# Performance work log

Hardware: AMD Instinct MI355X
Metric: run time of the kernel (lower is better)

The kernel has to match this reference:

```python
import jax, jax.numpy as jnp
import numpy as np

B, T, D = 2, 2048, 1024
H = 16
DH = D // H


def setup_inputs() -> dict:
    key = jax.random.key(0)
    ks = jax.random.split(key, 6)
    s = 1.0 / np.sqrt(D)
    return {
        "x": jax.random.normal(ks[0], (B, T, D), dtype=jnp.float32),
        "Wq": jax.random.normal(ks[1], (D, D), dtype=jnp.float32) * s,
        "Wk": jax.random.normal(ks[2], (D, D), dtype=jnp.float32) * s,
        "Wv": jax.random.normal(ks[3], (D, D), dtype=jnp.float32) * s,
        "Wo": jax.random.normal(ks[4], (D, D), dtype=jnp.float32) * s,
        "bo": jax.random.normal(ks[5], (D,), dtype=jnp.float32) * s,
    }


def reference(x, Wq, Wk, Wv, Wo, bo):
    b, t, _ = x.shape
    # separate Q/K/V projections (nn.Linear: x @ W.T, no bias)
    q = (x @ Wq.T).reshape(b, t, H, DH).transpose(0, 2, 1, 3)  # [b,h,t,hd]
    k = (x @ Wk.T).reshape(b, t, H, DH).transpose(0, 2, 1, 3)
    v = (x @ Wv.T).reshape(b, t, H, DH).transpose(0, 2, 1, 3)

    scores = jnp.einsum("bhqd,bhkd->bhqk", q, k)  # [b,h,t,t]
    causal = jnp.triu(jnp.ones((t, t), dtype=bool), k=1)
    scores = jnp.where(causal, -jnp.inf, scores)
    weights = jax.nn.softmax(scores / np.sqrt(DH), axis=-1)
    # dropout p=0.0 -> identity
    ctx = jnp.einsum("bhqk,bhkd->bhqd", weights, v)  # [b,h,t,hd]
    # NOTE: original code reshapes WITHOUT transposing heads back — replicate faithfully
    ctx = ctx.reshape(b, t, H * DH)
    return ctx @ Wo.T + bo
```

## Files before the change

### kernel.cpp

```cpp
#include <hip/hip_runtime.h>
#include <math.h>

#define BATCH 2
#define SEQ   2048
#define DIM   1024
#define NH    16
#define HD    64
#define MTOT  4096

typedef __attribute__((ext_vector_type(8)))  short bf16x8;
typedef __attribute__((ext_vector_type(4)))  float f32x4;
typedef __attribute__((ext_vector_type(16))) float f32x16;

__device__ __forceinline__ ushort f2bf(float f) {
    union { float f; unsigned u; } v; v.f = f;
    unsigned r = v.u + 0x7fffu + ((v.u >> 16) & 1u);
    return (ushort)(r >> 16);
}

__device__ __forceinline__ unsigned cvtpk_bf16(float lo, float hi) {
    unsigned r;
    asm("v_cvt_pk_bf16_f32 %0, %1, %2" : "=v"(r) : "v"(lo), "v"(hi));
    return r;
}

__global__ __launch_bounds__(256)
void cast_all(const float* __restrict__ x,
              const float* __restrict__ Wq, const float* __restrict__ Wk,
              const float* __restrict__ Wv, const float* __restrict__ Wo,
              ushort* __restrict__ xb,
              ushort* __restrict__ wqb, ushort* __restrict__ wkb,
              ushort* __restrict__ wvb, ushort* __restrict__ wob)
{
    const int z = blockIdx.y;
    const float* s; ushort* d; int n4;
    if (z == 0)      { s = x;  d = xb;  n4 = MTOT * DIM / 4; }
    else if (z == 1) { s = Wq; d = wqb; n4 = DIM * DIM / 4; }
    else if (z == 2) { s = Wk; d = wkb; n4 = DIM * DIM / 4; }
    else if (z == 3) { s = Wv; d = wvb; n4 = DIM * DIM / 4; }
    else             { s = Wo; d = wob; n4 = DIM * DIM / 4; }
    for (int i = blockIdx.x * blockDim.x + threadIdx.x; i < n4;
         i += gridDim.x * blockDim.x) {
        float4 v = ((const float4*)s)[i];
        ushort4 o;
        o.x = f2bf(v.x); o.y = f2bf(v.y); o.z = f2bf(v.z); o.w = f2bf(v.w);
        ((ushort4*)d)[i] = o;
    }
}

template<int MODE>
__global__ __launch_bounds__(256)
void gemm_bf16(const ushort* __restrict__ A,
               const ushort* __restrict__ W0, const ushort* __restrict__ W1,
               const ushort* __restrict__ W2,
               ushort* __restrict__ D0, ushort* __restrict__ D1,
               ushort* __restrict__ D2,
               const float* __restrict__ bias, float* __restrict__ Fout)
{
    __shared__ __align__(16) ushort As[2][128 * 64];
    __shared__ __align__(16) ushort Bs[2][128 * 64];

    const int tid = threadIdx.x;
    const int w = tid >> 6, l = tid & 63;
    const int g = l >> 4, l15 = l & 15;
    const int wr = w >> 1, wc = w & 1;
    const int brow = blockIdx.x * 128, bcol = blockIdx.y * 128;

    const ushort* W = (MODE == 1) ? W0
                    : (blockIdx.z == 0 ? W0 : (blockIdx.z == 1 ? W1 : W2));
    ushort* Dst = (MODE == 1) ? (ushort*)0
                : (blockIdx.z == 0 ? D0 : (blockIdx.z == 1 ? D1 : D2));

    const int rsub = l >> 3;
    const int gc   = ((l & 7) ^ rsub) * 8;
    const size_t arow0 = (size_t)(brow + 32 * w + rsub) * DIM;
    const size_t brow0 = (size_t)(bcol + 32 * w + rsub) * DIM;

    auto STAGE = [&](int buf, int ktel) {
        #pragma unroll
        for (int i = 0; i < 4; ++i) {
            __builtin_amdgcn_global_load_lds(
                (const __attribute__((address_space(1))) void*)
                    &A[arow0 + (size_t)(8 * i) * DIM + ktel + gc],
                (__attribute__((address_space(3))) void*)
                    &As[buf][(32 * w + 8 * i) * 64], 16, 0, 0);
            __builtin_amdgcn_global_load_lds(
                (const __attribute__((address_space(1))) void*)
                    &W[brow0 + (size_t)(8 * i) * DIM + ktel + gc],
                (__attribute__((address_space(3))) void*)
                    &Bs[buf][(32 * w + 8 * i) * 64], 16, 0, 0);
        }
    };

    STAGE(0, 0);
    STAGE(1, 64);

    f32x4 acc[4][4] = {};

    for (int t = 0; t < 16; ++t) {
        const int cur = t & 1;
        if (t < 15) asm volatile("s_waitcnt vmcnt(8)" ::: "memory");
        else        asm volatile("s_waitcnt vmcnt(0)" ::: "memory");
        __builtin_amdgcn_s_barrier();
        __builtin_amdgcn_sched_barrier(0);

        #pragma unroll
        for (int kh = 0; kh < 2; ++kh) {
            bf16x8 af[4], bfr[4];
            #pragma unroll
            for (int mi = 0; mi < 4; ++mi) {
                int row = 64 * wr + 16 * mi + l15;
                af[mi] = *(const bf16x8*)&As[cur][row * 64 + (((4 * kh + g) ^ (row & 7)) * 8)];
            }
            #pragma unroll
            for (int nj = 0; nj < 4; ++nj) {
                int row = 64 * wc + 16 * nj + l15;
                bfr[nj] = *(const bf16x8*)&Bs[cur][row * 64 + (((4 * kh + g) ^ (row & 7)) * 8)];
            }
            __builtin_amdgcn_s_setprio(1);
            #pragma unroll
            for (int mi = 0; mi < 4; ++mi)
                #pragma unroll
                for (int nj = 0; nj < 4; ++nj)
                    acc[mi][nj] = __builtin_amdgcn_mfma_f32_16x16x32_bf16(
                        af[mi], bfr[nj], acc[mi][nj], 0, 0, 0);
            __builtin_amdgcn_s_setprio(0);
        }

        __builtin_amdgcn_sched_barrier(0);
        __builtin_amdgcn_s_barrier();
        if (t + 2 < 16) STAGE(cur, (t + 2) * 64);
    }

    if (MODE == 0) {
        const float osc = (blockIdx.z == 0) ? 0.125f : 1.0f;
        if (blockIdx.z == 2) {
            #pragma unroll
            for (int mi = 0; mi < 4; ++mi)
                #pragma unroll
                for (int nj = 0; nj < 4; ++nj)
                    #pragma unroll
                    for (int reg = 0; reg < 4; ++reg) {
                        int row = brow + 64 * wr + 16 * mi + 4 * g + reg;
                        int col = bcol + 64 * wc + 16 * nj + l15;
                        int b = row >> 11, t = row & (SEQ - 1);
                        int hh = col >> 6, hd = col & 63;
                        Dst[(size_t)(b * NH + hh) * SEQ * HD
                            + ((size_t)(t >> 3) * 64 + hd) * 8 + (t & 7)] =
                            f2bf(acc[mi][nj][reg]);
                    }
        } else {
            #pragma unroll
            for (int mi = 0; mi < 4; ++mi)
                #pragma unroll
                for (int nj = 0; nj < 4; ++nj)
                    #pragma unroll
                    for (int reg = 0; reg < 4; ++reg) {
                        int row = brow + 64 * wr + 16 * mi + 4 * g + reg;
                        int col = bcol + 64 * wc + 16 * nj + l15;
                        int b = row >> 11, t = row & (SEQ - 1);
                        int hh = col >> 6, hd = col & 63;
                        Dst[(size_t)(b * NH + hh) * SEQ * HD
                            + (((size_t)(t >> 5) * 8 + (hd >> 3)) * 32 + (t & 31)) * 8
                            + (hd & 7)] = f2bf(acc[mi][nj][reg] * osc);
                    }
        }
    } else {
        #pragma unroll
        for (int nj = 0; nj < 4; ++nj) {
            int col = bcol + 64 * wc + 16 * nj + l15;
            float bv = bias[col];
            #pragma unroll
            for (int mi = 0; mi < 4; ++mi)
                #pragma unroll
                for (int reg = 0; reg < 4; ++reg) {
                    int row = brow + 64 * wr + 16 * mi + 4 * g + reg;
                    Fout[(size_t)row * DIM + col] = acc[mi][nj][reg] + bv;
                }
        }
    }
}

__global__ __launch_bounds__(256, 2)
void attn_mfma7(const ushort* __restrict__ q, const ushort* __restrict__ k,
                const ushort* __restrict__ vt, ushort* __restrict__ ctx)
{
    __shared__ float Olds[4 * 2048];
    __shared__ float Mlds[4][32];
    __shared__ float Llds[4][32];

    const int tid = threadIdx.x;
    const int wq = tid >> 6, l = tid & 63;
    const int l31 = l & 31, h = l >> 5;
    const int bh = blockIdx.x;
    const int qt = 63 - (int)blockIdx.y;
    const int qlo = qt * 32;
    const int nt  = (qt >> 1) + 1;
    const int cnt = (nt + 3) >> 2;
    const int kt0 = wq * cnt;
    const int kt1 = min(nt, kt0 + cnt);
    const float LOG2E = 1.44269504f;

    const ushort* Qg = q  + (size_t)bh * SEQ * HD;
    const ushort* Kg = k  + (size_t)bh * SEQ * HD;
    const ushort* Vg = vt + (size_t)bh * SEQ * HD;

    bf16x8 qf[4];
    #pragma unroll
    for (int s = 0; s < 4; ++s)
        qf[s] = *(const bf16x8*)&Qg[(((size_t)qt * 8 + 2 * s + h) * 32 + l31) * 8];

    f32x16 o[2] = {};
    float m = -3.0e38f, lsum = 0.f;

    if (kt0 < kt1) {
        bf16x8 kfA[8], kfB[8], vfA[8], vfB[8];
        #pragma unroll
        for (int s = 0; s < 4; ++s)
            #pragma unroll
            for (int f = 0; f < 2; ++f)
                kfA[2 * s + f] = *(const bf16x8*)
                    &Kg[(((size_t)(2 * kt0 + f) * 8 + 2 * s + h) * 32 + l31) * 8];
        #pragma unroll
        for (int s4 = 0; s4 < 4; ++s4)
            #pragma unroll
            for (int dt = 0; dt < 2; ++dt)
                vfA[2 * s4 + dt] = *(const bf16x8*)
                    &Vg[(((size_t)(8 * kt0 + 2 * s4 + h)) * 64 + 32 * dt + l31) * 8];

        auto body = [&](bf16x8 (&kc)[8], bf16x8 (&kn)[8],
                        bf16x8 (&vc)[8], bf16x8 (&vn)[8], int kt) {
            const int kvb = 64 * kt;

            f32x16 st[2] = {};
            #pragma unroll
            for (int s = 0; s < 4; ++s)
                #pragma unroll
                for (int f = 0; f < 2; ++f)
                    st[f] = __builtin_amdgcn_mfma_f32_32x32x16_bf16(
                        kc[2 * s + f], qf[s], st[f], 0, 0, 0);

            if (kt + 1 < kt1) {
                #pragma unroll
                for (int s = 0; s < 4; ++s)
                    #pragma unroll
                    for (int f = 0; f < 2; ++f)
                        kn[2 * s + f] = *(const bf16x8*)
                            &Kg[(((size_t)(2 * kt + 2 + f) * 8 + 2 * s + h) * 32 + l31) * 8];
                #pragma unroll
                for (int s4 = 0; s4 < 4; ++s4)
                    #pragma unroll
                    for (int dt = 0; dt < 2; ++dt)
                        vn[2 * s4 + dt] = *(const bf16x8*)
                            &Vg[(((size_t)(8 * kt + 8 + 2 * s4 + h)) * 64 + 32 * dt + l31) * 8];
            }

            const int qg = qlo + l31;
            if (kvb + 63 > qlo) {
                #pragma unroll
                for (int f = 0; f < 2; ++f)
                    #pragma unroll
                    for (int r = 0; r < 16; ++r) {
                        int kvg = kvb + 32 * f + (r & 3) + 8 * (r >> 2) + 4 * h;
                        if (kvg > qg) st[f][r] = -INFINITY;
                    }
            }

            float mx[8];
            #pragma unroll
            for (int i2 = 0; i2 < 8; ++i2) {
                const int f = i2 >> 2, rb = 4 * (i2 & 3);
                mx[i2] = fmaxf(fmaxf(st[f][rb], st[f][rb + 1]),
                               fmaxf(st[f][rb + 2], st[f][rb + 3]));
            }
            float tmax = fmaxf(fmaxf(fmaxf(mx[0], mx[1]), fmaxf(mx[2], mx[3])),
                               fmaxf(fmaxf(mx[4], mx[5]), fmaxf(mx[6], mx[7])));
            tmax = fmaxf(tmax, __shfl_xor(tmax, 32));
            float ty = fmaxf(tmax * LOG2E, -3.0e38f);

            if (!__all(ty - m <= 8.0f)) {
                float mn = fmaxf(m, ty);
                float sc = exp2f(m - mn);
                lsum *= sc;
                #pragma unroll
                for (int dt = 0; dt < 2; ++dt)
                    #pragma unroll
                    for (int r = 0; r < 16; ++r) o[dt][r] *= sc;
                m = mn;
            }

            float ls0 = 0.f, ls1 = 0.f, ls2 = 0.f, ls3 = 0.f;
            #pragma unroll
            for (int f = 0; f < 2; ++f)
                #pragma unroll
                for (int r = 0; r < 16; ++r) {
                    float pv = exp2f(fmaf(st[f][r], LOG2E, -m));
                    st[f][r] = pv;
                    if ((r & 3) == 0) ls0 += pv;
                    else if ((r & 3) == 1) ls1 += pv;
                    else if ((r & 3) == 2) ls2 += pv;
                    else ls3 += pv;
                }
            lsum += (ls0 + ls1) + (ls2 + ls3);

            #pragma unroll
            for (int s4 = 0; s4 < 4; ++s4) {
                const int f = s4 >> 1, rb2 = 8 * (s4 & 1);
                unsigned Aa = cvtpk_bf16(st[f][rb2 + 0], st[f][rb2 + 1]);
                unsigned Bb = cvtpk_bf16(st[f][rb2 + 2], st[f][rb2 + 3]);
                unsigned Cc = cvtpk_bf16(st[f][rb2 + 4], st[f][rb2 + 5]);
                unsigned Dd = cvtpk_bf16(st[f][rb2 + 6], st[f][rb2 + 7]);
                unsigned Ax = (unsigned)__shfl_xor((int)Aa, 32);
                unsigned Bx = (unsigned)__shfl_xor((int)Bb, 32);
                unsigned Cx = (unsigned)__shfl_xor((int)Cc, 32);
                unsigned Dx = (unsigned)__shfl_xor((int)Dd, 32);
                union { unsigned wv[4]; bf16x8 v; } pu;
                pu.wv[0] = h ? Cx : Aa;
                pu.wv[1] = h ? Dx : Bb;
                pu.wv[2] = h ? Cc : Ax;
                pu.wv[3] = h ? Dd : Bx;
                #pragma unroll
                for (int dt = 0; dt < 2; ++dt)
                    o[dt] = __builtin_amdgcn_mfma_f32_32x32x16_bf16(
                        vc[2 * s4 + dt], pu.v, o[dt], 0, 0, 0);
            }
        };

        int kt = kt0;
        while (true) {
            body(kfA, kfB, vfA, vfB, kt);
            if (++kt >= kt1) break;
            body(kfB, kfA, vfB, vfA, kt);
            if (++kt >= kt1) break;
        }
    }

    float lt = lsum + __shfl_xor(lsum, 32);
    if (h == 0) Mlds[wq][l31] = m;
    __syncthreads();
    float ms = fmaxf(fmaxf(Mlds[0][l31], Mlds[1][l31]),
                     fmaxf(Mlds[2][l31], Mlds[3][l31]));
    float fw = exp2f(m - ms);
    if (h == 0) Llds[wq][l31] = lt * fw;
    #pragma unroll
    for (int dt = 0; dt < 2; ++dt)
        #pragma unroll
        for (int r = 0; r < 16; ++r) {
            int d = 32 * dt + (r & 3) + 8 * (r >> 2) + 4 * h;
            Olds[wq * 2048 + d * 32 + (l31 ^ (d & 31))] = o[dt][r] * fw;
        }
    __syncthreads();

    const int tq = tid >> 3, tc = tid & 7;
    float inv = 1.0f / (Llds[0][tq] + Llds[1][tq] + Llds[2][tq] + Llds[3][tq]);
    union { ushort u[8]; int4 v4; } ov;
    #pragma unroll
    for (int i = 0; i < 8; i += 2) {
        int d0 = 8 * tc + i, d1 = d0 + 1;
        float s0 = 0.f, s1 = 0.f;
        #pragma unroll
        for (int ww = 0; ww < 4; ++ww) {
            s0 += Olds[ww * 2048 + d0 * 32 + (tq ^ (d0 & 31))];
            s1 += Olds[ww * 2048 + d1 * 32 + (tq ^ (d1 & 31))];
        }
        *(unsigned*)&ov.u[i] = cvtpk_bf16(s0 * inv, s1 * inv);
    }
    ushort* Cg = ctx + (size_t)bh * SEQ * HD + (size_t)qlo * HD;
    *(int4*)&Cg[tq * 64 + 8 * tc] = ov.v4;
}

extern "C" void kernel_launch(void* const* d_in, const int* in_sizes, int n_in,
                              void* d_out, int out_size, void* d_ws, size_t ws_size,
                              hipStream_t stream)
{
    (void)in_sizes; (void)n_in; (void)out_size; (void)ws_size;
    const float* x  = (const float*)d_in[0];
    const float* Wq = (const float*)d_in[1];
    const float* Wk = (const float*)d_in[2];
    const float* Wv = (const float*)d_in[3];
    const float* Wo = (const float*)d_in[4];
    const float* bo = (const float*)d_in[5];
    float* out = (float*)d_out;

    ushort* wsu  = (ushort*)d_ws;
    ushort* xb   = wsu;
    ushort* wqb  = wsu + 4194304;
    ushort* wkb  = wsu + 5242880;
    ushort* wvb  = wsu + 6291456;
    ushort* wob  = wsu + 7340032;
    ushort* qbuf = wsu + 8388608;
    ushort* kbuf = wsu + 12582912;
    ushort* vtb  = wsu + 16777216;
    ushort* ctxb = wsu + 20971520;

    cast_all<<<dim3(512, 5), 256, 0, stream>>>(x, Wq, Wk, Wv, Wo,
                                               xb, wqb, wkb, wvb, wob);

    dim3 gqkv(MTOT / 128, DIM / 128, 3);
    gemm_bf16<0><<<gqkv, 256, 0, stream>>>(xb, wqb, wkb, wvb,
                                           qbuf, kbuf, vtb, nullptr, nullptr);

    dim3 ga(BATCH * NH, SEQ / 32);
    attn_mfma7<<<ga, 256, 0, stream>>>(qbuf, kbuf, vtb, ctxb);

    dim3 go(MTOT / 128, DIM / 128, 1);
    gemm_bf16<1><<<go, 256, 0, stream>>>(ctxb, wob, nullptr, nullptr,
                                         nullptr, nullptr, nullptr, bo, out);
}
```

Before: 110.8 us.

## Stage QKV epilogue through LDS for coalesced stores; use permlane32_swap in attention

The QKV GEMM epilogue now writes bf16 results into shared memory in the target tiled layout, then issues coalesced 16-byte global stores, replacing scattered 2-byte stores. The attention kernel replaces the cross-half __shfl_xor exchanges with permlane32_swap for the P-matrix repack and the row-max reduction. It also raises wave priority around the MFMA blocks. This adds a barrier and LDS reuse in the GEMM epilogue, and it depends on the staging buffer being large enough and on the layout index math being correct.

```diff
diff --git a/kernel.cpp b/kernel.cpp
--- a/kernel.cpp
+++ b/kernel.cpp
@@ -11,6 +11,7 @@
 typedef __attribute__((ext_vector_type(8)))  short bf16x8;
 typedef __attribute__((ext_vector_type(4)))  float f32x4;
 typedef __attribute__((ext_vector_type(16))) float f32x16;
+typedef __attribute__((ext_vector_type(2)))  unsigned u32x2;
 
 __device__ __forceinline__ ushort f2bf(float f) {
     union { float f; unsigned u; } v; v.f = f;
@@ -133,37 +134,52 @@
     }
 
     if (MODE == 0) {
-        const float osc = (blockIdx.z == 0) ? 0.125f : 1.0f;
+        ushort* LB = (ushort*)As;
+        const int bB = brow >> 11, t0 = brow & (SEQ - 1);
         if (blockIdx.z == 2) {
+            #pragma unroll
+            for (int mi = 0; mi < 4; ++mi)
+                #pragma unroll
+                for (int nj = 0; nj < 4; ++nj) {
+                    int tlb = 64 * wr + 16 * mi + 4 * g;
+                    int hd = 16 * nj + l15;
+                    int sI = (tlb >> 3) * 2 + wc;
+                    uint2 pk;
+                    pk.x = cvtpk_bf16(acc[mi][nj][0], acc[mi][nj][1]);
+                    pk.y = cvtpk_bf16(acc[mi][nj][2], acc[mi][nj][3]);
+                    *(uint2*)&LB[sI * 512 + hd * 8 + (tlb & 7)] = pk;
+                }
+            __syncthreads();
+            #pragma unroll
+            for (int j = 0; j < 8; ++j) {
+                int4 v = *(const int4*)&LB[(j * 256 + tid) * 8];
+                int sI = j * 4 + (tid >> 6);
+                size_t base = (size_t)(bB * NH + 2 * blockIdx.y + (sI & 1)) * (SEQ * HD)
+                            + (size_t)((t0 >> 3) + (sI >> 1)) * 512 + (tid & 63) * 8;
+                *(int4*)&Dst[base] = v;
+            }
+        } else {
+            const float osc = (blockIdx.z == 0) ? 0.125f : 1.0f;
             #pragma unroll
             for (int mi = 0; mi < 4; ++mi)
                 #pragma unroll
                 for (int nj = 0; nj < 4; ++nj)
                     #pragma unroll
                     for (int reg = 0; reg < 4; ++reg) {
-                        int row = brow + 64 * wr + 16 * mi + 4 * g + reg;
-                        int col = bcol + 64 * wc + 16 * nj + l15;
-                        int b = row >> 11, t = row & (SEQ - 1);
-                        int hh = col >> 6, hd = col & 63;
-                        Dst[(size_t)(b * NH + hh) * SEQ * HD
-                            + ((size_t)(t >> 3) * 64 + hd) * 8 + (t & 7)] =
-                            f2bf(acc[mi][nj][reg]);
+                        int tl = 64 * wr + 16 * mi + 4 * g + reg;
+                        int hd = 16 * nj + l15;
+                        int sI = (tl >> 5) * 2 + wc;
+                        LB[sI * 2048 + (hd >> 3) * 256 + (tl & 31) * 8 + (hd & 7)] =
+                            f2bf(acc[mi][nj][reg] * osc);
                     }
-        } else {
-            #pragma unroll
-            for (int mi = 0; mi < 4; ++mi)
-                #pragma unroll
-                for (int nj = 0; nj < 4; ++nj)
-                    #pragma unroll
-                    for (int reg = 0; reg < 4; ++reg) {
-                        int row = brow + 64 * wr + 16 * mi + 4 * g + reg;
-                        int col = bcol + 64 * wc + 16 * nj + l15;
-                        int b = row >> 11, t = row & (SEQ - 1);
-                        int hh = col >> 6, hd = col & 63;
-                        Dst[(size_t)(b * NH + hh) * SEQ * HD
-                            + (((size_t)(t >> 5) * 8 + (hd >> 3)) * 32 + (t & 31)) * 8
-                            + (hd & 7)] = f2bf(acc[mi][nj][reg] * osc);
-                    }
+            __syncthreads();
+            #pragma unroll
+            for (int j = 0; j < 8; ++j) {
+                int4 v = *(const int4*)&LB[(j * 256 + tid) * 8];
+                size_t base = (size_t)(bB * NH + 2 * blockIdx.y + (j & 1)) * (SEQ * HD)
+                            + (size_t)((t0 >> 5) + (j >> 1)) * 2048 + tid * 8;
+                *(int4*)&Dst[base] = v;
+            }
         }
     } else {
         #pragma unroll
@@ -182,7 +198,7 @@
 }
 
 __global__ __launch_bounds__(256, 2)
-void attn_mfma7(const ushort* __restrict__ q, const ushort* __restrict__ k,
+void attn_mfma8(const ushort* __restrict__ q, const ushort* __restrict__ k,
                 const ushort* __restrict__ vt, ushort* __restrict__ ctx)
 {
     __shared__ float Olds[4 * 2048];
@@ -233,12 +249,14 @@
             const int kvb = 64 * kt;
 
             f32x16 st[2] = {};
+            __builtin_amdgcn_s_setprio(1);
             #pragma unroll
             for (int s = 0; s < 4; ++s)
                 #pragma unroll
                 for (int f = 0; f < 2; ++f)
                     st[f] = __builtin_amdgcn_mfma_f32_32x32x16_bf16(
                         kc[2 * s + f], qf[s], st[f], 0, 0, 0);
+            __builtin_amdgcn_s_setprio(0);
 
             if (kt + 1 < kt1) {
                 #pragma unroll
@@ -275,7 +293,12 @@
             }
             float tmax = fmaxf(fmaxf(fmaxf(mx[0], mx[1]), fmaxf(mx[2], mx[3])),
                                fmaxf(fmaxf(mx[4], mx[5]), fmaxf(mx[6], mx[7])));
-            tmax = fmaxf(tmax, __shfl_xor(tmax, 32));
+            {
+                union { float f; unsigned u; } tm; tm.f = tmax;
+                u32x2 ts = __builtin_amdgcn_permlane32_swap(tm.u, tm.u, false, false);
+                union { unsigned u; float f; } to; to.u = h ? ts.x : ts.y;
+                tmax = fmaxf(tmax, to.f);
+            }
             float ty = fmaxf(tmax * LOG2E, -3.0e38f);
 
             if (!__all(ty - m <= 8.0f)) {
@@ -310,19 +333,19 @@
                 unsigned Bb = cvtpk_bf16(st[f][rb2 + 2], st[f][rb2 + 3]);
                 unsigned Cc = cvtpk_bf16(st[f][rb2 + 4], st[f][rb2 + 5]);
                 unsigned Dd = cvtpk_bf16(st[f][rb2 + 6], st[f][rb2 + 7]);
-                unsigned Ax = (unsigned)__shfl_xor((int)Aa, 32);
-                unsigned Bx = (unsigned)__shfl_xor((int)Bb, 32);
-                unsigned Cx = (unsigned)__shfl_xor((int)Cc, 32);
-                unsigned Dx = (unsigned)__shfl_xor((int)Dd, 32);
+                u32x2 r02 = __builtin_amdgcn_permlane32_swap(Aa, Cc, false, false);
+                u32x2 r13 = __builtin_amdgcn_permlane32_swap(Bb, Dd, false, false);
                 union { unsigned wv[4]; bf16x8 v; } pu;
-                pu.wv[0] = h ? Cx : Aa;
-                pu.wv[1] = h ? Dx : Bb;
-                pu.wv[2] = h ? Cc : Ax;
-                pu.wv[3] = h ? Dd : Bx;
+                pu.wv[0] = r02.x;
+                pu.wv[1] = r13.x;
+                pu.wv[2] = r02.y;
+                pu.wv[3] = r13.y;
+                __builtin_amdgcn_s_setprio(1);
                 #pragma unroll
                 for (int dt = 0; dt < 2; ++dt)
                     o[dt] = __builtin_amdgcn_mfma_f32_32x32x16_bf16(
                         vc[2 * s4 + dt], pu.v, o[dt], 0, 0, 0);
+                __builtin_amdgcn_s_setprio(0);
             }
         };
 
@@ -401,7 +424,7 @@
                                            qbuf, kbuf, vtb, nullptr, nullptr);
 
     dim3 ga(BATCH * NH, SEQ / 32);
-    attn_mfma7<<<ga, 256, 0, stream>>>(qbuf, kbuf, vtb, ctxb);
+    attn_mfma8<<<ga, 256, 0, stream>>>(qbuf, kbuf, vtb, ctxb);
 
     dim3 go(MTOT / 128, DIM / 128, 1);
     gemm_bf16<1><<<go, 256, 0, stream>>>(ctxb, wob, nullptr, nullptr,
```

After: 107.8 us. 2.7% less time.
